# Kernel optimization log

Hardware: AMD Instinct MI355X
Metric: run time of the kernel (lower is better)

## Reference

```python
import jax, jax.numpy as jnp
import numpy as np
from jax import lax

N_QUBITS = 4
N_QLAYERS = 2
C64 = jnp.complex64
PAIRS = [(i, j) for i in range(N_QUBITS) for j in range(i + 1, N_QUBITS)]  # 6 entangling pairs
CNOT = jnp.array([[1, 0, 0, 0], [0, 1, 0, 0], [0, 0, 0, 1], [0, 0, 1, 0]], dtype=C64)


def _rx(t):
    c = jnp.cos(t / 2).astype(C64)
    s = (-1j * jnp.sin(t / 2)).astype(C64)
    return jnp.stack([jnp.stack([c, s]), jnp.stack([s, c])])


def _ry(t):
    c = jnp.cos(t / 2).astype(C64)
    s = jnp.sin(t / 2).astype(C64)
    return jnp.stack([jnp.stack([c, -s]), jnp.stack([s, c])])


def _rz(t):
    e = jnp.exp(-1j * t.astype(C64) / 2)
    z = jnp.zeros_like(e)
    return jnp.stack([jnp.stack([e, z]), jnp.stack([z, jnp.conj(e)])])


def _apply_1q(state, M, w):
    # state: (B,2,2,2,2); M: (2,2) shared or (B,2,2) per-sample
    s = jnp.moveaxis(state, 1 + w, -1)
    if M.ndim == 2:
        s = jnp.einsum('b...j,ij->b...i', s, M)
    else:
        s = jnp.einsum('b...j,bij->b...i', s, M)
    return jnp.moveaxis(s, -1, 1 + w)


def _apply_2q(state, M4, c, t):
    # M4: (4,4) acting on (wire c, wire t)
    s = jnp.moveaxis(state, (1 + c, 1 + t), (-2, -1))
    sh = s.shape
    s = s.reshape(sh[:-2] + (4,))
    s = jnp.einsum('b...j,ij->b...i', s, M4)
    s = s.reshape(sh)
    return jnp.moveaxis(s, (-2, -1), (1 + c, 1 + t))


def _quantum_batched(angles, q_params):
    # angles: (B, 4) classical outputs; encoding is RY(angles*pi)
    B = angles.shape[0]
    state = jnp.zeros((B, 16), C64).at[:, 0].set(1.0).reshape(B, 2, 2, 2, 2)
    theta = angles * jnp.float32(np.pi)
    c = jnp.cos(theta / 2).astype(C64)  # (B,4)
    s = jnp.sin(theta / 2).astype(C64)
    for w in range(N_QUBITS):
        M = jnp.stack([jnp.stack([c[:, w], -s[:, w]], -1),
                       jnp.stack([s[:, w], c[:, w]], -1)], -2)  # (B,2,2)
        state = _apply_1q(state, M, w)
    per_layer = 3 * N_QUBITS + len(PAIRS)  # 18
    for l in range(N_QLAYERS):
        start = l * per_layer
        rot = q_params[start:start + 3 * N_QUBITS].reshape(N_QUBITS, 3)
        ent = q_params[start + 3 * N_QUBITS:start + per_layer]
        for q in range(N_QUBITS):
            M = _rz(rot[q, 2]) @ _ry(rot[q, 1]) @ _rx(rot[q, 0])
            state = _apply_1q(state, M, q)
        for k, (i, j) in enumerate(PAIRS):
            M4 = jnp.kron(jnp.eye(2, dtype=C64), _rz(ent[k])) @ CNOT  # CNOT then RZ on target
            state = _apply_2q(state, M4, i, j)
    probs = jnp.abs(state) ** 2  # (B,2,2,2,2)
    signs = jnp.array([1.0, -1.0], jnp.float32)
    zs = []
    for w in range(N_QUBITS):
        pw = jnp.moveaxis(probs, 1 + w, -1).reshape(B, -1, 2)
        zs.append((pw.sum(1) * signs).sum(-1))
    return jnp.stack(zs, -1)  # (B,4) PauliZ expvals


def _conv(x, w, b):
    y = lax.conv_general_dilated(x, w, (1, 1), ((1, 1), (1, 1)),
                                 dimension_numbers=('NCHW', 'OIHW', 'NCHW'))
    return y + b[None, :, None, None]


def _pool(x):
    return lax.reduce_window(x, -jnp.inf, lax.max, (1, 1, 2, 2), (1, 1, 2, 2), 'VALID')


def setup_inputs() -> dict:
    key = jax.random.key(0)
    ks = jax.random.split(key, 10)
    B = 4096
    return {
        'x': jax.random.normal(ks[0], (B, 1, 28, 28), jnp.float32),
        'conv1_w': jax.random.normal(ks[1], (16, 1, 3, 3), jnp.float32) * 0.1,
        'conv1_b': jax.random.normal(ks[2], (16,), jnp.float32) * 0.1,
        'conv2_w': jax.random.normal(ks[3], (32, 16, 3, 3), jnp.float32) * 0.05,
        'conv2_b': jax.random.normal(ks[4], (32,), jnp.float32) * 0.1,
        'dense_w': jax.random.normal(ks[5], (4, 1568), jnp.float32) * 0.02,
        'dense_b': jax.random.normal(ks[6], (4,), jnp.float32) * 0.1,
        'q_params': jax.random.normal(ks[7], (36,), jnp.float32) * 0.1,
        'post_w': jax.random.normal(ks[8], (10, 4), jnp.float32) * 0.5,
        'post_b': jax.random.normal(ks[9], (10,), jnp.float32) * 0.1,
    }


def reference(x, conv1_w, conv1_b, conv2_w, conv2_b, dense_w, dense_b, q_params, post_w, post_b):
    h = jax.nn.relu(_conv(x, conv1_w, conv1_b))
    h = _pool(h)
    h = jax.nn.relu(_conv(h, conv2_w, conv2_b))
    h = _pool(h)  # (B,32,7,7)
    h = h.reshape(h.shape[0], 32 * 7 * 7)
    # dropout is identity in eval mode
    angles = h @ dense_w.T + dense_b  # (B,4)
    z = _quantum_batched(angles, q_params)  # (B,4)
    return z @ post_w.T + post_b  # (B,10)
```

## Files before the change

kernel.cpp:

```cpp
#include <hip/hip_runtime.h>

#define PI_F 3.14159265358979323846f

typedef _Float16 half2v __attribute__((ext_vector_type(2)));
typedef _Float16 half4v __attribute__((ext_vector_type(4)));
typedef _Float16 half8v __attribute__((ext_vector_type(8)));
typedef float f32x4 __attribute__((ext_vector_type(4)));

struct C2 { float x, y; };
__device__ __forceinline__ C2 cmul(C2 a, C2 b) {
    return C2{a.x * b.x - a.y * b.y, a.x * b.y + a.y * b.x};
}

__device__ __forceinline__ void gate1(float& re, float& im, int l, int w,
                                      C2 m00, C2 m01, C2 m10, C2 m11) {
    int mask = 1 << (3 - w);
    float pre = __shfl_xor(re, mask, 64);
    float pim = __shfl_xor(im, mask, 64);
    bool b = (l & mask) != 0;
    C2 d = b ? m11 : m00;
    C2 o = b ? m10 : m01;
    float nre = d.x * re - d.y * im + o.x * pre - o.y * pim;
    float nim = d.x * im + d.y * re + o.x * pim + o.y * pre;
    re = nre; im = nim;
}

#define WS_C1B 2560
#define WS_DWT 2688
#define WS_GROT 8960
#define WS_GENT 9024

__global__ __launch_bounds__(256) void qnn_prep(
    const float* __restrict__ w1g, const float* __restrict__ w2g,
    const float* __restrict__ dwg, const float* __restrict__ qpg,
    float* __restrict__ ws)
{
    int t = threadIdx.x;
    for (int e = t; e < 640; e += 256) {
        int kstep = e >> 7, rem = e & 127;
        int ntile = rem >> 6, lane = rem & 63;
        int kq = lane >> 4, n = lane & 15;
        int oc = ntile * 16 + n;
        int pi = kstep * 2 + (kq >> 1);
        half8v h;
        #pragma unroll
        for (int jj = 0; jj < 8; ++jj) {
            int ic = (kq & 1) * 8 + jj;
            float v = (pi < 9) ? w2g[oc * 144 + ic * 9 + pi] : 0.f;
            h[jj] = (_Float16)v;
        }
        *(float4*)(ws + e * 4) = __builtin_bit_cast(float4, h);
    }
    if (t < 64) {
        int ky = t >> 4, n = t & 15;
        half4v h;
        #pragma unroll
        for (int j = 0; j < 4; ++j) {
            float v = (ky < 3 && j < 3) ? w1g[n * 9 + ky * 3 + j] : 0.f;
            h[j] = (_Float16)v;
        }
        *(float2*)(ws + WS_C1B + t * 2) = __builtin_bit_cast(float2, h);
    }
    for (int e = t; e < 1568; e += 256) {
        float4 v = {dwg[e], dwg[1568 + e], dwg[3136 + e], dwg[4704 + e]};
        *(float4*)(ws + WS_DWT + e * 4) = v;
    }
    if (t < 8) {
        int layer = t >> 2, q = t & 3;
        int st = layer * 18;
        float a0 = qpg[st + 3 * q], a1 = qpg[st + 3 * q + 1], a2 = qpg[st + 3 * q + 2];
        float cx = cosf(0.5f * a0), sx = sinf(0.5f * a0);
        float cy = cosf(0.5f * a1), sy = sinf(0.5f * a1);
        float cz = cosf(0.5f * a2), sz = sinf(0.5f * a2);
        C2 T00{cy * cx,  sy * sx}, T01{-sy * cx, -cy * sx};
        C2 T10{sy * cx, -cy * sx}, T11{ cy * cx, -sy * sx};
        C2 E0{cz, -sz}, E1{cz, sz};
        C2 m00 = cmul(E0, T00), m01 = cmul(E0, T01);
        C2 m10 = cmul(E1, T10), m11 = cmul(E1, T11);
        float* gm = ws + WS_GROT + t * 8;
        gm[0] = m00.x; gm[1] = m00.y; gm[2] = m01.x; gm[3] = m01.y;
        gm[4] = m10.x; gm[5] = m10.y; gm[6] = m11.x; gm[7] = m11.y;
    }
    if (t >= 32 && t < 44) {
        int k = t - 32;
        float e = qpg[(k / 6) * 18 + 12 + (k % 6)];
        ws[WS_GENT + k * 2]     = cosf(0.5f * e);
        ws[WS_GENT + k * 2 + 1] = sinf(0.5f * e);
    }
}

__global__ __launch_bounds__(256, 6) void qnn_fused(
    const float* __restrict__ xg,
    const float* __restrict__ b1g, const float* __restrict__ b2g,
    const float* __restrict__ dbg,
    const float* __restrict__ wsc,
    const float* __restrict__ pwg, const float* __restrict__ pbg,
    float* __restrict__ out)
{
    const int b = blockIdx.x;
    const int t = threadIdx.x;
    const int lane = t & 63;
    const int wv = __builtin_amdgcn_readfirstlane(t >> 6);
    const int kq = lane >> 4;
    const int lm = lane & 15;

    __shared__ __align__(16) unsigned xhl[930];
    __shared__ __align__(16) _Float16 p1f[16 * 20 * 16];
    __shared__ __align__(16) float angp[16];

    half8v bC2[5][2];
    {
        const float4* wsB = (const float4*)wsc;
        #pragma unroll
        for (int ks = 0; ks < 5; ++ks)
            #pragma unroll
            for (int nt = 0; nt < 2; ++nt)
                bC2[ks][nt] = __builtin_bit_cast(half8v, wsB[(ks * 2 + nt) * 64 + lane]);
    }
    half4v bC1 = __builtin_bit_cast(half4v, *(const float2*)(wsc + WS_C1B + lane * 2));
    float bias1 = b1g[lm];
    float b20 = b2g[lm], b21 = b2g[16 + lm];

    const float* xb = xg + (size_t)b * 784;
    for (int j = t; j < 900; j += 256) {
        int y = j / 30, x = j - y * 30;
        float v = 0.f;
        if (y >= 1 && y <= 28 && x >= 1 && x <= 28)
            v = xb[(y - 1) * 28 + (x - 1)];
        _Float16 h = (_Float16)v;
        _Float16 l = (_Float16)(v - (float)h);
        half2v p; p.x = h; p.y = l;
        xhl[j] = __builtin_bit_cast(unsigned, p);
    }
    if (t < 30) xhl[900 + t] = 0u;
    {
        uint4 z4 = {0u, 0u, 0u, 0u};
        uint4* p4 = (uint4*)p1f;
        #pragma unroll
        for (int j = 0; j < 3; ++j) {
            int i = t + j * 256;
            if (i < 640) p4[i] = z4;
        }
    }
    __syncthreads();

    {
        int kyc = (kq < 3) ? kq : 0;
        int pos = lm & 3;
        int pyo = pos >> 1, pxo = pos & 1;
        int p14 = wv * 4 + (lm >> 2);
        int Y = p14 / 14, X = p14 - Y * 14;
        int q14 = wv * 4 + kq;
        int r = q14 / 14, c = q14 - r * 14;
        for (int tile = wv; tile < 49; tile += 4) {
            int py = 2 * Y + pyo, px = 2 * X + pxo;
            int base = (py + kyc) * 30 + px;
            unsigned u0 = xhl[base], u1 = xhl[base + 1], u2 = xhl[base + 2], u3 = xhl[base + 3];
            half2v h0 = __builtin_bit_cast(half2v, u0);
            half2v h1 = __builtin_bit_cast(half2v, u1);
            half2v h2 = __builtin_bit_cast(half2v, u2);
            half2v h3 = __builtin_bit_cast(half2v, u3);
            half4v ah = {h0.x, h1.x, h2.x, h3.x};
            half4v al = {h0.y, h1.y, h2.y, h3.y};
            f32x4 acc = {bias1, bias1, bias1, bias1};
            acc = __builtin_amdgcn_mfma_f32_16x16x16f16(ah, bC1, acc, 0, 0, 0);
            acc = __builtin_amdgcn_mfma_f32_16x16x16f16(al, bC1, acc, 0, 0, 0);
            float v = fmaxf(fmaxf(acc.x, acc.y), fmaxf(acc.z, acc.w));
            v = fmaxf(v, 0.f);
            p1f[((r + 1) * 20 + (c + 1)) * 16 + lm] = (_Float16)v;
            X += 2; Y += 1; if (X >= 14) { X -= 14; Y += 1; }
            c += 2; r += 1; if (c >= 14) { c -= 14; r += 1; }
        }
    }
    __syncthreads();

    {
        float dp0 = 0.f, dp1 = 0.f, dp2 = 0.f, dp3 = 0.f;
        const float4* dt = (const float4*)(wsc + WS_DWT);
        for (int tile = wv; tile < 13; tile += 4) {
            int m = tile * 16 + lm;
            int quad = m >> 2; if (quad > 48) quad = 48;
            int pos = m & 3;
            int Y = quad / 7, X = quad - Y * 7;
            int py = 2 * Y + (pos >> 1), px = 2 * X + (pos & 1);
            int base0 = py * 20 + px;
            f32x4 acc0 = {b20, b20, b20, b20};
            f32x4 acc1 = {b21, b21, b21, b21};
            int ich = (kq & 1) * 8;
            #pragma unroll
            for (int ks = 0; ks < 5; ++ks) {
                int pi = ks * 2 + (kq >> 1);
                if (pi > 8) pi = 8;
                int ky = (pi >= 6) ? 2 : ((pi >= 3) ? 1 : 0);
                int kx = pi - ky * 3;
                half8v a = *(const half8v*)(&p1f[(base0 + ky * 20 + kx) * 16 + ich]);
                acc0 = __builtin_amdgcn_mfma_f32_16x16x32_f16(a, bC2[ks][0], acc0, 0, 0, 0);
                acc1 = __builtin_amdgcn_mfma_f32_16x16x32_f16(a, bC2[ks][1], acc1, 0, 0, 0);
            }
            int quadO = tile * 4 + kq;
            if (quadO < 49) {
                float v0 = fmaxf(fmaxf(fmaxf(acc0.x, acc0.y), fmaxf(acc0.z, acc0.w)), 0.f);
                float v1 = fmaxf(fmaxf(fmaxf(acc1.x, acc1.y), fmaxf(acc1.z, acc1.w)), 0.f);
                float4 q0 = dt[lm * 49 + quadO];
                float4 q1 = dt[(16 + lm) * 49 + quadO];
                dp0 = fmaf(v0, q0.x, fmaf(v1, q1.x, dp0));
                dp1 = fmaf(v0, q0.y, fmaf(v1, q1.y, dp1));
                dp2 = fmaf(v0, q0.z, fmaf(v1, q1.z, dp2));
                dp3 = fmaf(v0, q0.w, fmaf(v1, q1.w, dp3));
            }
        }
        #pragma unroll
        for (int m = 32; m >= 1; m >>= 1) {
            dp0 += __shfl_xor(dp0, m, 64);
            dp1 += __shfl_xor(dp1, m, 64);
            dp2 += __shfl_xor(dp2, m, 64);
            dp3 += __shfl_xor(dp3, m, 64);
        }
        if (lane == 0) {
            float4 dpv = {dp0, dp1, dp2, dp3};
            *(float4*)&angp[wv * 4] = dpv;
        }
    }
    __syncthreads();

    if (t < 64) {
        float4 a0v = *(const float4*)&angp[0];
        float4 a1v = *(const float4*)&angp[4];
        float4 a2v = *(const float4*)&angp[8];
        float4 a3v = *(const float4*)&angp[12];
        float aw[4] = {a0v.x + a1v.x + a2v.x + a3v.x + dbg[0],
                       a0v.y + a1v.y + a2v.y + a3v.y + dbg[1],
                       a0v.z + a1v.z + a2v.z + a3v.z + dbg[2],
                       a0v.w + a1v.w + a2v.w + a3v.w + dbg[3]};
        int l = t & 15;
        float re = (l == 0) ? 1.f : 0.f;
        float im = 0.f;
        #pragma unroll
        for (int w = 0; w < 4; ++w) {
            float th = aw[w] * (PI_F * 0.5f);
            float c = cosf(th), s = sinf(th);
            gate1(re, im, l, w, C2{c, 0.f}, C2{-s, 0.f}, C2{s, 0.f}, C2{c, 0.f});
        }
        #pragma unroll
        for (int layer = 0; layer < 2; ++layer) {
            #pragma unroll
            for (int q = 0; q < 4; ++q) {
                const float* gm = wsc + WS_GROT + (layer * 4 + q) * 8;
                gate1(re, im, l, q, C2{gm[0], gm[1]}, C2{gm[2], gm[3]},
                                     C2{gm[4], gm[5]}, C2{gm[6], gm[7]});
            }
            const int pi_[6] = {0, 0, 0, 1, 1, 2};
            const int pj_[6] = {1, 2, 3, 2, 3, 3};
            #pragma unroll
            for (int k = 0; k < 6; ++k) {
                int i = pi_[k], j = pj_[k];
                const float* em = wsc + WS_GENT + (layer * 6 + k) * 2;
                float ce = em[0], se = em[1];
                int maskj = 1 << (3 - j);
                float pre = __shfl_xor(re, maskj, 64);
                float pim = __shfl_xor(im, maskj, 64);
                bool bi = ((l >> (3 - i)) & 1) != 0;
                re = bi ? pre : re;
                im = bi ? pim : im;
                bool bj = (l & maskj) != 0;
                C2 ph{ce, bj ? se : -se};
                C2 r = cmul(C2{re, im}, ph);
                re = r.x; im = r.y;
            }
        }
        float pr = re * re + im * im;
        float z0 = ((l >> 3) & 1) ? -pr : pr;
        float z1 = ((l >> 2) & 1) ? -pr : pr;
        float z2 = ((l >> 1) & 1) ? -pr : pr;
        float z3 = (l & 1)        ? -pr : pr;
        #pragma unroll
        for (int m = 1; m <= 8; m <<= 1) {
            z0 += __shfl_xor(z0, m, 64);
            z1 += __shfl_xor(z1, m, 64);
            z2 += __shfl_xor(z2, m, 64);
            z3 += __shfl_xor(z3, m, 64);
        }
        if (t < 10) {
            float4 pw4 = *(const float4*)(pwg + t * 4);
            float o = pbg[t];
            o = fmaf(z0, pw4.x, o); o = fmaf(z1, pw4.y, o);
            o = fmaf(z2, pw4.z, o); o = fmaf(z3, pw4.w, o);
            out[(size_t)b * 10 + t] = o;
        }
    }
}

extern "C" void kernel_launch(void* const* d_in, const int* in_sizes, int n_in,
                              void* d_out, int out_size, void* d_ws, size_t ws_size,
                              hipStream_t stream) {
    const float* x  = (const float*)d_in[0];
    const float* w1 = (const float*)d_in[1];
    const float* b1 = (const float*)d_in[2];
    const float* w2 = (const float*)d_in[3];
    const float* b2 = (const float*)d_in[4];
    const float* dw = (const float*)d_in[5];
    const float* db = (const float*)d_in[6];
    const float* qp = (const float*)d_in[7];
    const float* pw = (const float*)d_in[8];
    const float* pb = (const float*)d_in[9];
    float* out = (float*)d_out;
    float* ws  = (float*)d_ws;
    int B = in_sizes[0] / 784;

    qnn_prep<<<1, 256, 0, stream>>>(w1, w2, dw, qp, ws);
    qnn_fused<<<B, 256, 0, stream>>>(x, b1, b2, db, ws, pw, pb, out);
}
```

Measured before the change: 116.8 us.

## Process four samples per block and reorder dense weight layout

Each block now handles four batch samples in sequence, so the per-block setup (loading conv2 B fragments into registers, biases, padding zeroing) is paid once per four images, and the quantum stage runs all four samples in parallel, one per wavefront. The dense weight table is re-laid out quad-major so the per-quad float4 loads are contiguous across lanes. LDS rows are padded (stride 40 for input, 24 halves per p1f pixel), presumably to reduce bank conflicts, and conv1 now loads three taps instead of four. The trade-off is a quarter as many blocks, a lower occupancy hint, and a serial loop with three barriers per sample, which may reduce latency hiding.

New measurement: 117.9 us. Within noise of the previous version (+1.0%).

```diff
diff --git a/kernel.cpp b/kernel.cpp
--- a/kernel.cpp
+++ b/kernel.cpp
@@ -62,7 +62,9 @@
         *(float2*)(ws + WS_C1B + t * 2) = __builtin_bit_cast(float2, h);
     }
     for (int e = t; e < 1568; e += 256) {
-        float4 v = {dwg[e], dwg[1568 + e], dwg[3136 + e], dwg[4704 + e]};
+        int quad = e >> 5, oc = e & 31;
+        int src = oc * 49 + quad;
+        float4 v = {dwg[src], dwg[1568 + src], dwg[3136 + src], dwg[4704 + src]};
         *(float4*)(ws + WS_DWT + e * 4) = v;
     }
     if (t < 8) {
@@ -89,24 +91,24 @@
     }
 }
 
-__global__ __launch_bounds__(256, 6) void qnn_fused(
+__global__ __launch_bounds__(256, 4) void qnn_fused(
     const float* __restrict__ xg,
     const float* __restrict__ b1g, const float* __restrict__ b2g,
     const float* __restrict__ dbg,
     const float* __restrict__ wsc,
     const float* __restrict__ pwg, const float* __restrict__ pbg,
-    float* __restrict__ out)
+    float* __restrict__ out, int Btot)
 {
-    const int b = blockIdx.x;
+    const int b4 = blockIdx.x << 2;
     const int t = threadIdx.x;
     const int lane = t & 63;
     const int wv = __builtin_amdgcn_readfirstlane(t >> 6);
     const int kq = lane >> 4;
     const int lm = lane & 15;
 
-    __shared__ __align__(16) unsigned xhl[930];
-    __shared__ __align__(16) _Float16 p1f[16 * 20 * 16];
-    __shared__ __align__(16) float angp[16];
+    __shared__ __align__(16) unsigned xhl[1200];
+    __shared__ __align__(16) _Float16 p1f[16 * 20 * 24];
+    __shared__ __align__(16) float angp[64];
 
     half8v bC2[5][2];
     {
@@ -121,125 +123,136 @@
     float bias1 = b1g[lm];
     float b20 = b2g[lm], b21 = b2g[16 + lm];
 
-    const float* xb = xg + (size_t)b * 784;
-    for (int j = t; j < 900; j += 256) {
-        int y = j / 30, x = j - y * 30;
-        float v = 0.f;
-        if (y >= 1 && y <= 28 && x >= 1 && x <= 28)
-            v = xb[(y - 1) * 28 + (x - 1)];
-        _Float16 h = (_Float16)v;
-        _Float16 l = (_Float16)(v - (float)h);
-        half2v p; p.x = h; p.y = l;
-        xhl[j] = __builtin_bit_cast(unsigned, p);
-    }
-    if (t < 30) xhl[900 + t] = 0u;
     {
         uint4 z4 = {0u, 0u, 0u, 0u};
         uint4* p4 = (uint4*)p1f;
         #pragma unroll
-        for (int j = 0; j < 3; ++j) {
+        for (int j = 0; j < 4; ++j) {
             int i = t + j * 256;
-            if (i < 640) p4[i] = z4;
-        }
-    }
-    __syncthreads();
+            if (i < 960) p4[i] = z4;
+        }
+    }
+
+    for (int e = 0; e < 4; ++e) {
+        const int bi = b4 + e;
+        {
+            const float* xb = xg + (size_t)bi * 784;
+            int y = t / 40;
+            int x = t - y * 40;
+            #pragma unroll
+            for (int it = 0; it < 5; ++it) {
+                int j = t + it * 256;
+                if (j < 1200) {
+                    float v = 0.f;
+                    if (bi < Btot && y >= 1 && y <= 28 && x >= 1 && x <= 28)
+                        v = xb[y * 28 + x - 29];
+                    _Float16 h = (_Float16)v;
+                    _Float16 lo = (_Float16)(v - (float)h);
+                    half2v p; p.x = h; p.y = lo;
+                    xhl[j] = __builtin_bit_cast(unsigned, p);
+                }
+                x += 16; y += 6; if (x >= 40) { x -= 40; y += 1; }
+            }
+        }
+        __syncthreads();
+
+        {
+            int kyc = (kq < 3) ? kq : 0;
+            int pos = lm & 3;
+            int pyo = pos >> 1, pxo = pos & 1;
+            int p14 = wv * 4 + (lm >> 2);
+            int Y = p14 / 14, X = p14 - Y * 14;
+            int q14 = wv * 4 + kq;
+            int r = q14 / 14, c = q14 - r * 14;
+            for (int tile = wv; tile < 49; tile += 4) {
+                int py = 2 * Y + pyo, px = 2 * X + pxo;
+                int base = (py + kyc) * 40 + px;
+                unsigned u0 = xhl[base], u1 = xhl[base + 1], u2 = xhl[base + 2];
+                half2v h0 = __builtin_bit_cast(half2v, u0);
+                half2v h1 = __builtin_bit_cast(half2v, u1);
+                half2v h2 = __builtin_bit_cast(half2v, u2);
+                half4v ah = {h0.x, h1.x, h2.x, (_Float16)0.f};
+                half4v al = {h0.y, h1.y, h2.y, (_Float16)0.f};
+                f32x4 acc = {bias1, bias1, bias1, bias1};
+                acc = __builtin_amdgcn_mfma_f32_16x16x16f16(ah, bC1, acc, 0, 0, 0);
+                acc = __builtin_amdgcn_mfma_f32_16x16x16f16(al, bC1, acc, 0, 0, 0);
+                float v = fmaxf(fmaxf(fmaxf(acc.x, acc.y), fmaxf(acc.z, acc.w)), 0.f);
+                p1f[((r + 1) * 20 + (c + 1)) * 24 + lm] = (_Float16)v;
+                X += 2; Y += 1; if (X >= 14) { X -= 14; Y += 1; }
+                c += 2; r += 1; if (c >= 14) { c -= 14; r += 1; }
+            }
+        }
+        __syncthreads();
+
+        {
+            float dp0 = 0.f, dp1 = 0.f, dp2 = 0.f, dp3 = 0.f;
+            const float4* dt = (const float4*)(wsc + WS_DWT);
+            for (int tile = wv; tile < 13; tile += 4) {
+                int m = tile * 16 + lm;
+                int quad = m >> 2; if (quad > 48) quad = 48;
+                int pos = m & 3;
+                int Y = quad / 7, X = quad - Y * 7;
+                int py = 2 * Y + (pos >> 1), px = 2 * X + (pos & 1);
+                int base0 = py * 20 + px;
+                f32x4 acc0 = {b20, b20, b20, b20};
+                f32x4 acc1 = {b21, b21, b21, b21};
+                int ich = (kq & 1) * 8;
+                #pragma unroll
+                for (int ks = 0; ks < 5; ++ks) {
+                    int pi = ks * 2 + (kq >> 1);
+                    if (pi > 8) pi = 8;
+                    int ky = (pi >= 6) ? 2 : ((pi >= 3) ? 1 : 0);
+                    int kx = pi - ky * 3;
+                    half8v a = *(const half8v*)(&p1f[(base0 + ky * 20 + kx) * 24 + ich]);
+                    acc0 = __builtin_amdgcn_mfma_f32_16x16x32_f16(a, bC2[ks][0], acc0, 0, 0, 0);
+                    acc1 = __builtin_amdgcn_mfma_f32_16x16x32_f16(a, bC2[ks][1], acc1, 0, 0, 0);
+                }
+                int quadO = tile * 4 + kq;
+                if (quadO < 49) {
+                    float v0 = fmaxf(fmaxf(fmaxf(acc0.x, acc0.y), fmaxf(acc0.z, acc0.w)), 0.f);
+                    float v1 = fmaxf(fmaxf(fmaxf(acc1.x, acc1.y), fmaxf(acc1.z, acc1.w)), 0.f);
+                    float4 q0 = dt[quadO * 32 + lm];
+                    float4 q1 = dt[quadO * 32 + 16 + lm];
+                    dp0 = fmaf(v0, q0.x, fmaf(v1, q1.x, dp0));
+                    dp1 = fmaf(v0, q0.y, fmaf(v1, q1.y, dp1));
+                    dp2 = fmaf(v0, q0.z, fmaf(v1, q1.z, dp2));
+                    dp3 = fmaf(v0, q0.w, fmaf(v1, q1.w, dp3));
+                }
+            }
+            #pragma unroll
+            for (int m = 32; m >= 1; m >>= 1) {
+                dp0 += __shfl_xor(dp0, m, 64);
+                dp1 += __shfl_xor(dp1, m, 64);
+                dp2 += __shfl_xor(dp2, m, 64);
+                dp3 += __shfl_xor(dp3, m, 64);
+            }
+            if (lane == 0) {
+                float4 dpv = {dp0, dp1, dp2, dp3};
+                *(float4*)&angp[e * 16 + wv * 4] = dpv;
+            }
+        }
+        __syncthreads();
+    }
 
     {
-        int kyc = (kq < 3) ? kq : 0;
-        int pos = lm & 3;
-        int pyo = pos >> 1, pxo = pos & 1;
-        int p14 = wv * 4 + (lm >> 2);
-        int Y = p14 / 14, X = p14 - Y * 14;
-        int q14 = wv * 4 + kq;
-        int r = q14 / 14, c = q14 - r * 14;
-        for (int tile = wv; tile < 49; tile += 4) {
-            int py = 2 * Y + pyo, px = 2 * X + pxo;
-            int base = (py + kyc) * 30 + px;
-            unsigned u0 = xhl[base], u1 = xhl[base + 1], u2 = xhl[base + 2], u3 = xhl[base + 3];
-            half2v h0 = __builtin_bit_cast(half2v, u0);
-            half2v h1 = __builtin_bit_cast(half2v, u1);
-            half2v h2 = __builtin_bit_cast(half2v, u2);
-            half2v h3 = __builtin_bit_cast(half2v, u3);
-            half4v ah = {h0.x, h1.x, h2.x, h3.x};
-            half4v al = {h0.y, h1.y, h2.y, h3.y};
-            f32x4 acc = {bias1, bias1, bias1, bias1};
-            acc = __builtin_amdgcn_mfma_f32_16x16x16f16(ah, bC1, acc, 0, 0, 0);
-            acc = __builtin_amdgcn_mfma_f32_16x16x16f16(al, bC1, acc, 0, 0, 0);
-            float v = fmaxf(fmaxf(acc.x, acc.y), fmaxf(acc.z, acc.w));
-            v = fmaxf(v, 0.f);
-            p1f[((r + 1) * 20 + (c + 1)) * 16 + lm] = (_Float16)v;
-            X += 2; Y += 1; if (X >= 14) { X -= 14; Y += 1; }
-            c += 2; r += 1; if (c >= 14) { c -= 14; r += 1; }
-        }
-    }
-    __syncthreads();
-
-    {
-        float dp0 = 0.f, dp1 = 0.f, dp2 = 0.f, dp3 = 0.f;
-        const float4* dt = (const float4*)(wsc + WS_DWT);
-        for (int tile = wv; tile < 13; tile += 4) {
-            int m = tile * 16 + lm;
-            int quad = m >> 2; if (quad > 48) quad = 48;
-            int pos = m & 3;
-            int Y = quad / 7, X = quad - Y * 7;
-            int py = 2 * Y + (pos >> 1), px = 2 * X + (pos & 1);
-            int base0 = py * 20 + px;
-            f32x4 acc0 = {b20, b20, b20, b20};
-            f32x4 acc1 = {b21, b21, b21, b21};
-            int ich = (kq & 1) * 8;
-            #pragma unroll
-            for (int ks = 0; ks < 5; ++ks) {
-                int pi = ks * 2 + (kq >> 1);
-                if (pi > 8) pi = 8;
-                int ky = (pi >= 6) ? 2 : ((pi >= 3) ? 1 : 0);
-                int kx = pi - ky * 3;
-                half8v a = *(const half8v*)(&p1f[(base0 + ky * 20 + kx) * 16 + ich]);
-                acc0 = __builtin_amdgcn_mfma_f32_16x16x32_f16(a, bC2[ks][0], acc0, 0, 0, 0);
-                acc1 = __builtin_amdgcn_mfma_f32_16x16x32_f16(a, bC2[ks][1], acc1, 0, 0, 0);
-            }
-            int quadO = tile * 4 + kq;
-            if (quadO < 49) {
-                float v0 = fmaxf(fmaxf(fmaxf(acc0.x, acc0.y), fmaxf(acc0.z, acc0.w)), 0.f);
-                float v1 = fmaxf(fmaxf(fmaxf(acc1.x, acc1.y), fmaxf(acc1.z, acc1.w)), 0.f);
-                float4 q0 = dt[lm * 49 + quadO];
-                float4 q1 = dt[(16 + lm) * 49 + quadO];
-                dp0 = fmaf(v0, q0.x, fmaf(v1, q1.x, dp0));
-                dp1 = fmaf(v0, q0.y, fmaf(v1, q1.y, dp1));
-                dp2 = fmaf(v0, q0.z, fmaf(v1, q1.z, dp2));
-                dp3 = fmaf(v0, q0.w, fmaf(v1, q1.w, dp3));
-            }
-        }
-        #pragma unroll
-        for (int m = 32; m >= 1; m >>= 1) {
-            dp0 += __shfl_xor(dp0, m, 64);
-            dp1 += __shfl_xor(dp1, m, 64);
-            dp2 += __shfl_xor(dp2, m, 64);
-            dp3 += __shfl_xor(dp3, m, 64);
-        }
-        if (lane == 0) {
-            float4 dpv = {dp0, dp1, dp2, dp3};
-            *(float4*)&angp[wv * 4] = dpv;
-        }
-    }
-    __syncthreads();
-
-    if (t < 64) {
-        float4 a0v = *(const float4*)&angp[0];
-        float4 a1v = *(const float4*)&angp[4];
-        float4 a2v = *(const float4*)&angp[8];
-        float4 a3v = *(const float4*)&angp[12];
+        const int bi = b4 + wv;
+        const float* ap = angp + wv * 16;
+        float4 a0v = *(const float4*)(ap);
+        float4 a1v = *(const float4*)(ap + 4);
+        float4 a2v = *(const float4*)(ap + 8);
+        float4 a3v = *(const float4*)(ap + 12);
         float aw[4] = {a0v.x + a1v.x + a2v.x + a3v.x + dbg[0],
                        a0v.y + a1v.y + a2v.y + a3v.y + dbg[1],
                        a0v.z + a1v.z + a2v.z + a3v.z + dbg[2],
                        a0v.w + a1v.w + a2v.w + a3v.w + dbg[3]};
-        int l = t & 15;
+        int l = lm;
         float re = (l == 0) ? 1.f : 0.f;
         float im = 0.f;
         #pragma unroll
         for (int w = 0; w < 4; ++w) {
             float th = aw[w] * (PI_F * 0.5f);
-            float c = cosf(th), s = sinf(th);
-            gate1(re, im, l, w, C2{c, 0.f}, C2{-s, 0.f}, C2{s, 0.f}, C2{c, 0.f});
+            float cth = cosf(th), sth = sinf(th);
+            gate1(re, im, l, w, C2{cth, 0.f}, C2{-sth, 0.f}, C2{sth, 0.f}, C2{cth, 0.f});
         }
         #pragma unroll
         for (int layer = 0; layer < 2; ++layer) {
@@ -259,13 +272,13 @@
                 int maskj = 1 << (3 - j);
                 float pre = __shfl_xor(re, maskj, 64);
                 float pim = __shfl_xor(im, maskj, 64);
-                bool bi = ((l >> (3 - i)) & 1) != 0;
-                re = bi ? pre : re;
-                im = bi ? pim : im;
+                bool ci = ((l >> (3 - i)) & 1) != 0;
+                re = ci ? pre : re;
+                im = ci ? pim : im;
                 bool bj = (l & maskj) != 0;
                 C2 ph{ce, bj ? se : -se};
-                C2 r = cmul(C2{re, im}, ph);
-                re = r.x; im = r.y;
+                C2 rr = cmul(C2{re, im}, ph);
+                re = rr.x; im = rr.y;
             }
         }
         float pr = re * re + im * im;
@@ -280,12 +293,12 @@
             z2 += __shfl_xor(z2, m, 64);
             z3 += __shfl_xor(z3, m, 64);
         }
-        if (t < 10) {
-            float4 pw4 = *(const float4*)(pwg + t * 4);
-            float o = pbg[t];
+        if (lane < 10 && bi < Btot) {
+            float4 pw4 = *(const float4*)(pwg + lane * 4);
+            float o = pbg[lane];
             o = fmaf(z0, pw4.x, o); o = fmaf(z1, pw4.y, o);
             o = fmaf(z2, pw4.z, o); o = fmaf(z3, pw4.w, o);
-            out[(size_t)b * 10 + t] = o;
+            out[(size_t)bi * 10 + lane] = o;
         }
     }
 }
@@ -306,7 +319,8 @@
     float* out = (float*)d_out;
     float* ws  = (float*)d_ws;
     int B = in_sizes[0] / 784;
+    int nb = (B + 3) >> 2;
 
     qnn_prep<<<1, 256, 0, stream>>>(w1, w2, dw, qp, ws);
-    qnn_fused<<<B, 256, 0, stream>>>(x, b1, b2, db, ws, pw, pb, out);
-}
+    qnn_fused<<<nb, 256, 0, stream>>>(x, b1, b2, db, ws, pw, pb, out, B);
+}
```
